# Kernel tuning notes

Measured on AMD Instinct MI355X. Metric: run time of the kernel, lower is better.

## Reference

```python
import jax, jax.numpy as jnp
import numpy as np

B, S, D, C = 64, 576, 768, 200


def setup_inputs() -> dict:
    key = jax.random.key(0)
    k1, k2, k3, k4 = jax.random.split(key, 4)
    return {
        "patch_tokens": jax.random.normal(k1, (B, S, D), dtype=jnp.float32),
        "class_token": jax.random.normal(k2, (B, D), dtype=jnp.float32),
        "attn_w": jax.random.normal(k3, (C, D), dtype=jnp.float32) * (1.0 / np.sqrt(D)),
        "attn_b": jnp.zeros((C,), dtype=jnp.float32),
        "gc_w": jax.random.normal(k4, (C, D), dtype=jnp.float32) * (1.0 / np.sqrt(D)),
        "gc_b": jnp.zeros((C,), dtype=jnp.float32),
        "lam": jnp.ones((1,), dtype=jnp.float32),
    }


def reference(patch_tokens, class_token, attn_w, attn_b, gc_w, gc_b, lam):
    # patch_tokens: (B,S,D). The torch module reshapes S to HxW, but the mean
    # over (H,W) equals the mean over S, so we stay in token layout.
    _, S_, D_ = patch_tokens.shape
    # Global classifier: (B,C)
    global_scores = class_token @ gc_w.T + gc_b
    # Per-class 1x1 conv == per-class linear projection over tokens: (B,C,S)
    att = jax.nn.sigmoid(
        jnp.einsum("bsd,cd->bcs", patch_tokens, attn_w) + attn_b[None, :, None]
    )
    # mean over spatial (S) then mean over channels (D):
    # mean_d mean_s (att * feat) == einsum / (S*D)
    attention_scores = jnp.einsum("bcs,bsd->bc", att, patch_tokens) / (S_ * D_)
    return global_scores + lam[0] * attention_scores
```

## Files before the change

kernel.cpp:

```cpp
#include <hip/hip_runtime.h>
#include <math.h>

#define Bsz  64
#define Ssz  576
#define Dsz  768
#define Csz  200
#define MT   48
#define NKT  12

typedef float f32x4 __attribute__((ext_vector_type(4)));
typedef long  lx2   __attribute__((ext_vector_type(2)));

__global__ __launch_bounds__(256) void prep_w8(const float* __restrict__ W,
                                               unsigned long long* __restrict__ Wq) {
    const int i  = blockIdx.x * 256 + threadIdx.x;
    const int h  = i & 1;
    const int j  = i >> 1;
    const int l  = j & 63;
    const int r2 = j >> 6;
    const int t  = r2 % 13;
    const int kt = r2 / 13;
    const int q  = l >> 4, m = l & 15;
    const int row = t * 16 + m;
    const int col = kt * 64 + h * 32 + ((q >> 1) << 4) + ((q & 1) << 3);
    unsigned long long v = 0ull;
    if (row < Csz) {
        const float4 a = *(const float4*)(W + (size_t)row * Dsz + col);
        const float4 b = *(const float4*)(W + (size_t)row * Dsz + col + 4);
        unsigned int lo = __builtin_amdgcn_cvt_pk_fp8_f32(a.x, a.y, 0u, false);
        lo = __builtin_amdgcn_cvt_pk_fp8_f32(a.z, a.w, lo, true);
        unsigned int hi = __builtin_amdgcn_cvt_pk_fp8_f32(b.x, b.y, 0u, false);
        hi = __builtin_amdgcn_cvt_pk_fp8_f32(b.z, b.w, hi, true);
        v = ((unsigned long long)hi << 32) | (unsigned long long)lo;
    } else if (row == Csz) {
        v = 0x3838383838383838ull;
    }
    Wq[i] = v;
}

__global__ __launch_bounds__(256) void gc_kernel(
    const float* __restrict__ ct, const float* __restrict__ gw,
    const float* __restrict__ gb, float* __restrict__ out) {
    const int b    = blockIdx.x;
    const int wv   = threadIdx.x >> 6;
    const int lane = threadIdx.x & 63;
    const int c    = blockIdx.y * 4 + wv;
    const float* wr = gw + (size_t)c * Dsz + lane * 12;
    const float* cr = ct + (size_t)b * Dsz + lane * 12;
    float s = 0.f;
#pragma unroll
    for (int j = 0; j < 3; ++j) {
        const float4 w = *(const float4*)(wr + 4 * j);
        const float4 x = *(const float4*)(cr + 4 * j);
        s += w.x * x.x + w.y * x.y + w.z * x.z + w.w * x.w;
    }
#pragma unroll
    for (int off = 32; off > 0; off >>= 1) s += __shfl_down(s, off, 64);
    if (lane == 0) out[b * Csz + c] = s + gb[c];
}

__device__ __forceinline__ long cvtA(const f32x4 lo, const f32x4 hi) {
    union { long l; unsigned int u[2]; } A;
    A.u[0] = __builtin_amdgcn_cvt_pk_fp8_f32(lo.x, lo.y, 0u, false);
    A.u[0] = __builtin_amdgcn_cvt_pk_fp8_f32(lo.z, lo.w, A.u[0], true);
    A.u[1] = __builtin_amdgcn_cvt_pk_fp8_f32(hi.x, hi.y, 0u, false);
    A.u[1] = __builtin_amdgcn_cvt_pk_fp8_f32(hi.z, hi.w, A.u[1], true);
    return A.l;
}

template<int KT>
__device__ __forceinline__ void body(f32x4 (&xs)[4], const float* xp,
                                     const unsigned char* wp, f32x4 (&acc)[13]) {
    lx2 wfa[7];
#pragma unroll
    for (int t = 0; t < 7; ++t)
        wfa[t] = *(const lx2*)(wp + (size_t)(KT * 13 + t) * 1024);
    const long A0 = cvtA(xs[0], xs[1]);
    const long A1 = cvtA(xs[2], xs[3]);
    if (KT + 3 < NKT) {
#pragma unroll
        for (int j = 0; j < 4; ++j)
            xs[j] = *(const f32x4*)(xp + (KT + 3) * 64 + (j >> 1) * 32 + (j & 1) * 4);
    }
#pragma unroll
    for (int t = 0; t < 7; ++t) {
        acc[t] = __builtin_amdgcn_mfma_f32_16x16x32_fp8_fp8(A0, wfa[t][0], acc[t], 0, 0, 0);
        acc[t] = __builtin_amdgcn_mfma_f32_16x16x32_fp8_fp8(A1, wfa[t][1], acc[t], 0, 0, 0);
    }
    lx2 wfb[6];
#pragma unroll
    for (int t = 0; t < 6; ++t)
        wfb[t] = *(const lx2*)(wp + (size_t)(KT * 13 + 7 + t) * 1024);
#pragma unroll
    for (int t = 0; t < 6; ++t) {
        acc[7 + t] = __builtin_amdgcn_mfma_f32_16x16x32_fp8_fp8(A0, wfb[t][0], acc[7 + t], 0, 0, 0);
        acc[7 + t] = __builtin_amdgcn_mfma_f32_16x16x32_fp8_fp8(A1, wfb[t][1], acc[7 + t], 0, 0, 0);
    }
}

__global__ __launch_bounds__(192, 3) void attn_kernel(
    const float* __restrict__ X,
    const unsigned char* __restrict__ Wq,
    const float* __restrict__ attn_b,
    const float* __restrict__ lam,
    float* __restrict__ out)
{
    const int tid  = threadIdx.x;
    const int lane = tid & 63;
    const int w    = tid >> 6;
    const int m    = lane & 15;
    const int q    = lane >> 4;
    const int rowbase = blockIdx.x * MT;
    const int bidx    = blockIdx.x / 12;

    const float* xp = X + (size_t)(rowbase + w * 16 + m) * Dsz + q * 8;
    const unsigned char* wp = Wq + lane * 16;

    f32x4 xA[4], xB[4], xC[4];
#pragma unroll
    for (int j = 0; j < 4; ++j)
        xA[j] = *(const f32x4*)(xp + 0 * 64 + (j >> 1) * 32 + (j & 1) * 4);
#pragma unroll
    for (int j = 0; j < 4; ++j)
        xB[j] = *(const f32x4*)(xp + 1 * 64 + (j >> 1) * 32 + (j & 1) * 4);
#pragma unroll
    for (int j = 0; j < 4; ++j)
        xC[j] = *(const f32x4*)(xp + 2 * 64 + (j >> 1) * 32 + (j & 1) * 4);

    f32x4 acc[13];
#pragma unroll
    for (int t = 0; t < 13; ++t) acc[t] = (f32x4){0.f, 0.f, 0.f, 0.f};

    body<0>(xA, xp, wp, acc);
    body<1>(xB, xp, wp, acc);
    body<2>(xC, xp, wp, acc);
    body<3>(xA, xp, wp, acc);
    body<4>(xB, xp, wp, acc);
    body<5>(xC, xp, wp, acc);
    body<6>(xA, xp, wp, acc);
    body<7>(xB, xp, wp, acc);
    body<8>(xC, xp, wp, acc);
    body<9>(xA, xp, wp, acc);
    body<10>(xB, xp, wp, acc);
    body<11>(xC, xp, wp, acc);

    float rsv[4];
#pragma unroll
    for (int r = 0; r < 4; ++r) rsv[r] = __shfl(acc[12][r], (lane & 48) + 8, 64);

    const float scale = lam[0] * (1.f / ((float)Ssz * (float)Dsz));
#pragma unroll
    for (int t = 0; t < 13; ++t) {
        const int c = t * 16 + m;
        if (c < Csz) {
            const float bias = attn_b[c];
            float s = 0.f;
#pragma unroll
            for (int r = 0; r < 4; ++r)
                s += rsv[r] / (1.f + __expf(-(acc[t][r] + bias)));
            s += __shfl_xor(s, 16, 64);
            s += __shfl_xor(s, 32, 64);
            if (q == 0) atomicAdd(&out[bidx * Csz + c], s * scale);
        }
    }
}

extern "C" void kernel_launch(void* const* d_in, const int* in_sizes, int n_in,
                              void* d_out, int out_size, void* d_ws, size_t ws_size,
                              hipStream_t stream) {
    const float* X   = (const float*)d_in[0];
    const float* ct  = (const float*)d_in[1];
    const float* aw  = (const float*)d_in[2];
    const float* ab  = (const float*)d_in[3];
    const float* gw  = (const float*)d_in[4];
    const float* gb  = (const float*)d_in[5];
    const float* lam = (const float*)d_in[6];
    float* out = (float*)d_out;
    unsigned long long* Wq = (unsigned long long*)d_ws;

    prep_w8<<<(NKT * 13 * 64 * 2) / 256, 256, 0, stream>>>(aw, Wq);
    gc_kernel<<<dim3(Bsz, Csz / 4), 256, 0, stream>>>(ct, gw, gb, out);
    attn_kernel<<<(Bsz * Ssz) / MT, 192, 0, stream>>>(X, (const unsigned char*)Wq, ab, lam, out);
}
```

Before: 208.0 us.

## Split K across four waves per 16-row tile with LDS reduction

Each block now handles 16 token rows instead of 48, and its four waves each take a quarter of the D dimension (three 64-wide K tiles). The partial accumulators are summed through shared memory in two stages before wave 0 runs the sigmoid-weighted epilogue. This gives more blocks and more independent waves, with all X loads issued up front, and adds s_setprio around the MFMA groups. The cost is LDS traffic, three barriers, an epilogue that runs on a single wave, and each block loading the full FP8 weight set for only 16 rows, which repeats weight traffic.

```diff
diff --git a/kernel.cpp b/kernel.cpp
--- a/kernel.cpp
+++ b/kernel.cpp
@@ -5,7 +5,6 @@
 #define Ssz  576
 #define Dsz  768
 #define Csz  200
-#define MT   48
 #define NKT  12
 
 typedef float f32x4 __attribute__((ext_vector_type(4)));
@@ -68,99 +67,116 @@
     return A.l;
 }
 
-template<int KT>
-__device__ __forceinline__ void body(f32x4 (&xs)[4], const float* xp,
-                                     const unsigned char* wp, f32x4 (&acc)[13]) {
-    lx2 wfa[7];
-#pragma unroll
-    for (int t = 0; t < 7; ++t)
-        wfa[t] = *(const lx2*)(wp + (size_t)(KT * 13 + t) * 1024);
-    const long A0 = cvtA(xs[0], xs[1]);
-    const long A1 = cvtA(xs[2], xs[3]);
-    if (KT + 3 < NKT) {
-#pragma unroll
-        for (int j = 0; j < 4; ++j)
-            xs[j] = *(const f32x4*)(xp + (KT + 3) * 64 + (j >> 1) * 32 + (j & 1) * 4);
-    }
-#pragma unroll
-    for (int t = 0; t < 7; ++t) {
-        acc[t] = __builtin_amdgcn_mfma_f32_16x16x32_fp8_fp8(A0, wfa[t][0], acc[t], 0, 0, 0);
-        acc[t] = __builtin_amdgcn_mfma_f32_16x16x32_fp8_fp8(A1, wfa[t][1], acc[t], 0, 0, 0);
-    }
-    lx2 wfb[6];
-#pragma unroll
-    for (int t = 0; t < 6; ++t)
-        wfb[t] = *(const lx2*)(wp + (size_t)(KT * 13 + 7 + t) * 1024);
-#pragma unroll
-    for (int t = 0; t < 6; ++t) {
-        acc[7 + t] = __builtin_amdgcn_mfma_f32_16x16x32_fp8_fp8(A0, wfb[t][0], acc[7 + t], 0, 0, 0);
-        acc[7 + t] = __builtin_amdgcn_mfma_f32_16x16x32_fp8_fp8(A1, wfb[t][1], acc[7 + t], 0, 0, 0);
-    }
-}
-
-__global__ __launch_bounds__(192, 3) void attn_kernel(
+__global__ __launch_bounds__(256, 4) void attn_kernel(
     const float* __restrict__ X,
     const unsigned char* __restrict__ Wq,
     const float* __restrict__ attn_b,
     const float* __restrict__ lam,
     float* __restrict__ out)
 {
+    __shared__ float sred[2][64][53];
+
     const int tid  = threadIdx.x;
     const int lane = tid & 63;
     const int w    = tid >> 6;
     const int m    = lane & 15;
     const int q    = lane >> 4;
-    const int rowbase = blockIdx.x * MT;
-    const int bidx    = blockIdx.x / 12;
-
-    const float* xp = X + (size_t)(rowbase + w * 16 + m) * Dsz + q * 8;
+    const int row0 = blockIdx.x * 16;
+    const int bidx = blockIdx.x / 36;
+
+    const float* xp = X + (size_t)(row0 + m) * Dsz + w * 192 + q * 8;
     const unsigned char* wp = Wq + lane * 16;
 
-    f32x4 xA[4], xB[4], xC[4];
-#pragma unroll
-    for (int j = 0; j < 4; ++j)
-        xA[j] = *(const f32x4*)(xp + 0 * 64 + (j >> 1) * 32 + (j & 1) * 4);
-#pragma unroll
-    for (int j = 0; j < 4; ++j)
-        xB[j] = *(const f32x4*)(xp + 1 * 64 + (j >> 1) * 32 + (j & 1) * 4);
-#pragma unroll
-    for (int j = 0; j < 4; ++j)
-        xC[j] = *(const f32x4*)(xp + 2 * 64 + (j >> 1) * 32 + (j & 1) * 4);
+    f32x4 xr[12];
+#pragma unroll
+    for (int kk = 0; kk < 3; ++kk) {
+#pragma unroll
+        for (int j = 0; j < 4; ++j)
+            xr[kk * 4 + j] = *(const f32x4*)(xp + kk * 64 + (j >> 1) * 32 + (j & 1) * 4);
+    }
 
     f32x4 acc[13];
 #pragma unroll
     for (int t = 0; t < 13; ++t) acc[t] = (f32x4){0.f, 0.f, 0.f, 0.f};
 
-    body<0>(xA, xp, wp, acc);
-    body<1>(xB, xp, wp, acc);
-    body<2>(xC, xp, wp, acc);
-    body<3>(xA, xp, wp, acc);
-    body<4>(xB, xp, wp, acc);
-    body<5>(xC, xp, wp, acc);
-    body<6>(xA, xp, wp, acc);
-    body<7>(xB, xp, wp, acc);
-    body<8>(xC, xp, wp, acc);
-    body<9>(xA, xp, wp, acc);
-    body<10>(xB, xp, wp, acc);
-    body<11>(xC, xp, wp, acc);
-
-    float rsv[4];
-#pragma unroll
-    for (int r = 0; r < 4; ++r) rsv[r] = __shfl(acc[12][r], (lane & 48) + 8, 64);
-
-    const float scale = lam[0] * (1.f / ((float)Ssz * (float)Dsz));
-#pragma unroll
-    for (int t = 0; t < 13; ++t) {
-        const int c = t * 16 + m;
-        if (c < Csz) {
-            const float bias = attn_b[c];
-            float s = 0.f;
-#pragma unroll
-            for (int r = 0; r < 4; ++r)
-                s += rsv[r] / (1.f + __expf(-(acc[t][r] + bias)));
-            s += __shfl_xor(s, 16, 64);
-            s += __shfl_xor(s, 32, 64);
-            if (q == 0) atomicAdd(&out[bidx * Csz + c], s * scale);
+#pragma unroll
+    for (int kk = 0; kk < 3; ++kk) {
+        const int kt = 3 * w + kk;
+        const long A0 = cvtA(xr[kk * 4 + 0], xr[kk * 4 + 1]);
+        const long A1 = cvtA(xr[kk * 4 + 2], xr[kk * 4 + 3]);
+        lx2 wfa[7];
+#pragma unroll
+        for (int t = 0; t < 7; ++t)
+            wfa[t] = *(const lx2*)(wp + (size_t)(kt * 13 + t) * 1024);
+        __builtin_amdgcn_s_setprio(1);
+#pragma unroll
+        for (int t = 0; t < 7; ++t) {
+            acc[t] = __builtin_amdgcn_mfma_f32_16x16x32_fp8_fp8(A0, wfa[t][0], acc[t], 0, 0, 0);
+            acc[t] = __builtin_amdgcn_mfma_f32_16x16x32_fp8_fp8(A1, wfa[t][1], acc[t], 0, 0, 0);
+        }
+        __builtin_amdgcn_s_setprio(0);
+        lx2 wfb[6];
+#pragma unroll
+        for (int t = 0; t < 6; ++t)
+            wfb[t] = *(const lx2*)(wp + (size_t)(kt * 13 + 7 + t) * 1024);
+        __builtin_amdgcn_s_setprio(1);
+#pragma unroll
+        for (int t = 0; t < 6; ++t) {
+            acc[7 + t] = __builtin_amdgcn_mfma_f32_16x16x32_fp8_fp8(A0, wfb[t][0], acc[7 + t], 0, 0, 0);
+            acc[7 + t] = __builtin_amdgcn_mfma_f32_16x16x32_fp8_fp8(A1, wfb[t][1], acc[7 + t], 0, 0, 0);
+        }
+        __builtin_amdgcn_s_setprio(0);
+    }
+
+    if (w >= 2) {
+#pragma unroll
+        for (int t = 0; t < 13; ++t) {
+#pragma unroll
+            for (int r = 0; r < 4; ++r) sred[w - 2][lane][t * 4 + r] = acc[t][r];
+        }
+    }
+    __syncthreads();
+    if (w < 2) {
+#pragma unroll
+        for (int t = 0; t < 13; ++t) {
+#pragma unroll
+            for (int r = 0; r < 4; ++r) acc[t][r] += sred[w][lane][t * 4 + r];
+        }
+    }
+    __syncthreads();
+    if (w == 1) {
+#pragma unroll
+        for (int t = 0; t < 13; ++t) {
+#pragma unroll
+            for (int r = 0; r < 4; ++r) sred[0][lane][t * 4 + r] = acc[t][r];
+        }
+    }
+    __syncthreads();
+
+    if (w == 0) {
+#pragma unroll
+        for (int t = 0; t < 13; ++t) {
+#pragma unroll
+            for (int r = 0; r < 4; ++r) acc[t][r] += sred[0][lane][t * 4 + r];
+        }
+        float rsv[4];
+#pragma unroll
+        for (int r = 0; r < 4; ++r) rsv[r] = __shfl(acc[12][r], (lane & 48) + 8, 64);
+
+        const float scale = lam[0] * (1.f / ((float)Ssz * (float)Dsz));
+#pragma unroll
+        for (int t = 0; t < 13; ++t) {
+            const int c = t * 16 + m;
+            if (c < Csz) {
+                const float bias = attn_b[c];
+                float s = 0.f;
+#pragma unroll
+                for (int r = 0; r < 4; ++r)
+                    s += rsv[r] / (1.f + __expf(-(acc[t][r] + bias)));
+                s += __shfl_xor(s, 16, 64);
+                s += __shfl_xor(s, 32, 64);
+                if (q == 0) atomicAdd(&out[bidx * Csz + c], s * scale);
+            }
         }
     }
 }
@@ -180,5 +196,5 @@
 
     prep_w8<<<(NKT * 13 * 64 * 2) / 256, 256, 0, stream>>>(aw, Wq);
     gc_kernel<<<dim3(Bsz, Csz / 4), 256, 0, stream>>>(ct, gw, gb, out);
-    attn_kernel<<<(Bsz * Ssz) / MT, 192, 0, stream>>>(X, (const unsigned char*)Wq, ab, lam, out);
-}
+    attn_kernel<<<(Bsz * Ssz) / 16, 256, 0, stream>>>(X, (const unsigned char*)Wq, ab, lam, out);
+}
```

Measured after the change: 197.0 us. 5.3% less time.

## Stage fp8 weights in LDS per block and deepen X prefetch pipeline

Applied to the files above, without the earlier changes.

Enlarges each attention block to 144 rows (9 waves) and copies the entire fp8-quantized weight matrix (156 KB) into shared memory once per block with global_load_lds. MFMA weight fragments are then read from LDS rather than re-fetched from global/L2 by every wave. X rows are prefetched four k-tiles ahead using inline-asm loads with explicit vmcnt waits. The 156 KB LDS footprint limits occupancy to one or two blocks per CU, and the hand-counted vmcnt values depend on exact load ordering, so a miscount could read stale data.

```diff
diff --git a/kernel.cpp b/kernel.cpp
--- a/kernel.cpp
+++ b/kernel.cpp
@@ -5,11 +5,19 @@
 #define Ssz  576
 #define Dsz  768
 #define Csz  200
-#define MT   48
+#define MTL  144
 #define NKT  12
 
 typedef float f32x4 __attribute__((ext_vector_type(4)));
 typedef long  lx2   __attribute__((ext_vector_type(2)));
+
+#define AS_GLOBAL __attribute__((address_space(1)))
+#define AS_LDS    __attribute__((address_space(3)))
+
+__device__ inline void gload16(const void* g, void* l) {
+    __builtin_amdgcn_global_load_lds((const AS_GLOBAL unsigned int*)g,
+                                     (AS_LDS unsigned int*)l, 16, 0, 0);
+}
 
 __global__ __launch_bounds__(256) void prep_w8(const float* __restrict__ W,
                                                unsigned long long* __restrict__ Wq) {
@@ -68,81 +76,88 @@
     return A.l;
 }
 
+#define XLOAD(g, KT) do {                                                        \
+    asm volatile("global_load_dwordx4 %0, %1, off offset:%2"                     \
+                 : "=v"(g[0]) : "v"(xp), "i"((KT) * 256 + 0));                   \
+    asm volatile("global_load_dwordx4 %0, %1, off offset:%2"                     \
+                 : "=v"(g[1]) : "v"(xp), "i"((KT) * 256 + 16));                  \
+    asm volatile("global_load_dwordx4 %0, %1, off offset:%2"                     \
+                 : "=v"(g[2]) : "v"(xp), "i"((KT) * 256 + 128));                 \
+    asm volatile("global_load_dwordx4 %0, %1, off offset:%2"                     \
+                 : "=v"(g[3]) : "v"(xp), "i"((KT) * 256 + 144));                 \
+} while (0)
+
 template<int KT>
-__device__ __forceinline__ void body(f32x4 (&xs)[4], const float* xp,
-                                     const unsigned char* wp, f32x4 (&acc)[13]) {
-    lx2 wfa[7];
-#pragma unroll
-    for (int t = 0; t < 7; ++t)
-        wfa[t] = *(const lx2*)(wp + (size_t)(KT * 13 + t) * 1024);
-    const long A0 = cvtA(xs[0], xs[1]);
-    const long A1 = cvtA(xs[2], xs[3]);
-    if (KT + 3 < NKT) {
-#pragma unroll
-        for (int j = 0; j < 4; ++j)
-            xs[j] = *(const f32x4*)(xp + (KT + 3) * 64 + (j >> 1) * 32 + (j & 1) * 4);
+__device__ __forceinline__ void body(f32x4 (&g)[4], const float* xp,
+                                     const unsigned char* swp, f32x4 (&acc)[13]) {
+    constexpr int NWAIT = (KT + 4 < NKT) ? 12 : 4 * (NKT - 1 - KT);
+    asm volatile("s_waitcnt vmcnt(%0)" :: "i"(NWAIT) : "memory");
+    __builtin_amdgcn_sched_barrier(0);
+    const long A0 = cvtA(g[0], g[1]);
+    const long A1 = cvtA(g[2], g[3]);
+    if constexpr (KT + 4 < NKT) {
+        XLOAD(g, KT + 4);
     }
 #pragma unroll
-    for (int t = 0; t < 7; ++t) {
-        acc[t] = __builtin_amdgcn_mfma_f32_16x16x32_fp8_fp8(A0, wfa[t][0], acc[t], 0, 0, 0);
-        acc[t] = __builtin_amdgcn_mfma_f32_16x16x32_fp8_fp8(A1, wfa[t][1], acc[t], 0, 0, 0);
-    }
-    lx2 wfb[6];
-#pragma unroll
-    for (int t = 0; t < 6; ++t)
-        wfb[t] = *(const lx2*)(wp + (size_t)(KT * 13 + 7 + t) * 1024);
-#pragma unroll
-    for (int t = 0; t < 6; ++t) {
-        acc[7 + t] = __builtin_amdgcn_mfma_f32_16x16x32_fp8_fp8(A0, wfb[t][0], acc[7 + t], 0, 0, 0);
-        acc[7 + t] = __builtin_amdgcn_mfma_f32_16x16x32_fp8_fp8(A1, wfb[t][1], acc[7 + t], 0, 0, 0);
+    for (int t = 0; t < 13; ++t) {
+        const lx2 wf = *(const lx2*)(swp + (KT * 13 + t) * 1024);
+        acc[t] = __builtin_amdgcn_mfma_f32_16x16x32_fp8_fp8(A0, wf[0], acc[t], 0, 0, 0);
+        acc[t] = __builtin_amdgcn_mfma_f32_16x16x32_fp8_fp8(A1, wf[1], acc[t], 0, 0, 0);
     }
 }
 
-__global__ __launch_bounds__(192, 3) void attn_kernel(
+__global__ __launch_bounds__(576, 2) void attn_kernel(
     const float* __restrict__ X,
     const unsigned char* __restrict__ Wq,
     const float* __restrict__ attn_b,
     const float* __restrict__ lam,
     float* __restrict__ out)
 {
+    __shared__ unsigned char sW[156 * 1024];
+
     const int tid  = threadIdx.x;
     const int lane = tid & 63;
     const int w    = tid >> 6;
     const int m    = lane & 15;
     const int q    = lane >> 4;
-    const int rowbase = blockIdx.x * MT;
-    const int bidx    = blockIdx.x / 12;
+    const int rowbase = blockIdx.x * MTL;
+    const int bidx    = blockIdx.x >> 2;
 
     const float* xp = X + (size_t)(rowbase + w * 16 + m) * Dsz + q * 8;
-    const unsigned char* wp = Wq + lane * 16;
+    const unsigned char* swp = sW + lane * 16;
 
-    f32x4 xA[4], xB[4], xC[4];
 #pragma unroll
-    for (int j = 0; j < 4; ++j)
-        xA[j] = *(const f32x4*)(xp + 0 * 64 + (j >> 1) * 32 + (j & 1) * 4);
-#pragma unroll
-    for (int j = 0; j < 4; ++j)
-        xB[j] = *(const f32x4*)(xp + 1 * 64 + (j >> 1) * 32 + (j & 1) * 4);
-#pragma unroll
-    for (int j = 0; j < 4; ++j)
-        xC[j] = *(const f32x4*)(xp + 2 * 64 + (j >> 1) * 32 + (j & 1) * 4);
+    for (int j = 0; j < 18; ++j) {
+        const int g = w * 18 + j;
+        if (g < 156) gload16(Wq + (size_t)g * 1024 + lane * 16, sW + g * 1024);
+    }
+
+    f32x4 xg0[4], xg1[4], xg2[4], xg3[4];
+    XLOAD(xg0, 0);
+    XLOAD(xg1, 1);
+    XLOAD(xg2, 2);
+    XLOAD(xg3, 3);
+
+    asm volatile("s_waitcnt vmcnt(16)" ::: "memory");
+    __builtin_amdgcn_sched_barrier(0);
+    asm volatile("s_barrier" ::: "memory");
 
     f32x4 acc[13];
 #pragma unroll
     for (int t = 0; t < 13; ++t) acc[t] = (f32x4){0.f, 0.f, 0.f, 0.f};
 
-    body<0>(xA, xp, wp, acc);
-    body<1>(xB, xp, wp, acc);
-    body<2>(xC, xp, wp, acc);
-    body<3>(xA, xp, wp, acc);
-    body<4>(xB, xp, wp, acc);
-    body<5>(xC, xp, wp, acc);
-    body<6>(xA, xp, wp, acc);
-    body<7>(xB, xp, wp, acc);
-    body<8>(xC, xp, wp, acc);
-    body<9>(xA, xp, wp, acc);
-    body<10>(xB, xp, wp, acc);
-    body<11>(xC, xp, wp, acc);
+    body<0>(xg0, xp, swp, acc);
+    body<1>(xg1, xp, swp, acc);
+    body<2>(xg2, xp, swp, acc);
+    body<3>(xg3, xp, swp, acc);
+    body<4>(xg0, xp, swp, acc);
+    body<5>(xg1, xp, swp, acc);
+    body<6>(xg2, xp, swp, acc);
+    body<7>(xg3, xp, swp, acc);
+    body<8>(xg0, xp, swp, acc);
+    body<9>(xg1, xp, swp, acc);
+    body<10>(xg2, xp, swp, acc);
+    body<11>(xg3, xp, swp, acc);
 
     float rsv[4];
 #pragma unroll
@@ -180,5 +195,5 @@
 
     prep_w8<<<(NKT * 13 * 64 * 2) / 256, 256, 0, stream>>>(aw, Wq);
     gc_kernel<<<dim3(Bsz, Csz / 4), 256, 0, stream>>>(ct, gw, gb, out);
-    attn_kernel<<<(Bsz * Ssz) / MT, 192, 0, stream>>>(X, (const unsigned char*)Wq, ab, lam, out);
+    attn_kernel<<<(Bsz * Ssz) / MTL, 576, 0, stream>>>(X, (const unsigned char*)Wq, ab, lam, out);
 }
```

Result: faster. 193.0 us (-7.2%).
